# Optimization experiments

Hardware: AMD Instinct MI355X
Metric: run time of the kernel (lower is better)

Reference implementation:

```python
import jax, jax.numpy as jnp
import numpy as np

N_HEAD = 12
MIN_SIZE = 4
MAX_SIZE = 8
TOP_M = 16
ALPHA = 1.0
EPS = 1e-6
NEG_INF = -1e30


def setup_inputs() -> dict:
    key = jax.random.key(0)
    ks = jax.random.split(key, 4)
    B, T, C = 2, 512, 768
    x = jax.random.normal(ks[0], (B, T, C), jnp.float32)
    w_qkv = jax.random.normal(ks[1], (C, 3 * C), jnp.float32) * (1.0 / np.sqrt(C))
    b_qkv = jnp.zeros((3 * C,), jnp.float32)
    w_proj = jax.random.normal(ks[2], (C, C), jnp.float32) * (1.0 / np.sqrt(C))
    b_proj = jnp.zeros((C,), jnp.float32)
    gate_param = jnp.zeros((), jnp.float32)  # dpp_gate_init = 0.0 -> gate = 0.5
    return {"x": x, "w_qkv": w_qkv, "b_qkv": b_qkv, "w_proj": w_proj,
            "b_proj": b_proj, "gate_param": gate_param}


def _dpp_token(i, q_i, k, v):
    """Greedy DPP subset selection + attention for one query token.
    q_i: [hd], k/v: [T, hd]. Faithful to the torch greedy loop, vectorized
    over candidates with incremental Gram construction (scores only gate the
    discrete selection, so they are computed under stop_gradient, matching
    torch where they only feed Python comparisons)."""
    T, hd = k.shape
    kc = jax.lax.stop_gradient(k)
    qc = jax.lax.stop_gradient(q_i)
    # causal similarity, topk candidates
    sim = jnp.where(jnp.arange(T) <= i, kc @ qc, NEG_INF)
    _, topidx = jax.lax.top_k(sim, TOP_M)  # [M]
    # candidates = top-min(TOP_M, i+1) causal neighbors, excluding i itself
    cand_active = (jnp.arange(TOP_M) < jnp.minimum(TOP_M, i + 1)) & (topidx != i)
    cand_keys = kc[topidx]                              # [M, hd]
    cnorm = jnp.sum(cand_keys * cand_keys, axis=-1)     # [M]

    sel_idx = jnp.zeros((MAX_SIZE,), jnp.int32).at[0].set(i)
    sel_count = jnp.int32(1)
    # initial score: log(det([k_i.k_i]) + eps) / 1**alpha
    cur = jnp.log(jnp.dot(kc[i], kc[i]) + EPS)
    stopped = jnp.bool_(False)
    eye = jnp.eye(MAX_SIZE, dtype=jnp.float32)
    slots = jnp.arange(MAX_SIZE)

    for _ in range(MAX_SIZE - 1):
        rowmask = slots < sel_count                       # [S] current subset rows
        pos = (slots == sel_count).astype(jnp.float32)    # slot for new candidate
        Ksel = kc[sel_idx] * rowmask[:, None].astype(jnp.float32)  # [S, hd]
        G0 = Ksel @ Ksel.T                                # [S, S]
        cross = cand_keys @ Ksel.T                        # [M, S]
        # Gc[c,a,b] = G0[a,b] + pos[a]*cross[c,b] + pos[b]*cross[c,a] + pos[a]pos[b]*cnorm[c]
        Gc = (G0[None]
              + pos[None, :, None] * cross[:, None, :]
              + pos[None, None, :] * cross[:, :, None]
              + (pos[:, None] * pos[None, :])[None] * cnorm[:, None, None])
        newmask = rowmask | (slots == sel_count)
        # identity-pad unused rows/cols so det equals det of the active submatrix
        Gc = Gc + (eye * (1.0 - newmask.astype(jnp.float32)))[None]
        dets = jnp.linalg.det(Gc)                         # [M] (float32, as torch)
        size = (sel_count + 1).astype(jnp.float32)
        score = jnp.log(dets + EPS) / size ** ALPHA       # minimize_det=False
        masked = jnp.where(cand_active, score, NEG_INF)
        best = jnp.argmax(masked)
        best_score = masked[best]
        any_cand = jnp.any(cand_active)
        take = any_cand & (~stopped) & ((best_score > cur) | (sel_count < MIN_SIZE))
        sel_idx = jnp.where(take, sel_idx.at[sel_count].set(topidx[best].astype(jnp.int32)), sel_idx)
        cand_active = jnp.where(take, cand_active.at[best].set(False), cand_active)
        cur = jnp.where(take, best_score, cur)
        sel_count = sel_count + take.astype(jnp.int32)
        stopped = stopped | (~take)

    # attention over the selected subset (gradients flow through k, v, q here)
    rowmask = slots < sel_count
    Ks = k[sel_idx]
    Vs = v[sel_idx]
    logits = jnp.where(rowmask, (Ks @ q_i) / np.float32(np.sqrt(hd)), NEG_INF)
    w = jax.nn.softmax(logits)
    return w @ Vs


def _forward(x, w_qkv, b_qkv, w_proj, b_proj, gate_param):
    B, T, C = x.shape
    hd = C // N_HEAD
    qkv = x @ w_qkv + b_qkv
    q, k, v = jnp.split(qkv, 3, axis=-1)

    def heads(t):  # [B,T,C] -> [B*NH, T, hd]
        return t.reshape(B, T, N_HEAD, hd).transpose(0, 2, 1, 3).reshape(B * N_HEAD, T, hd)

    q, k, v = heads(q), heads(k), heads(v)

    # standard causal softmax attention (flash path, dropout=0 at eval)
    scale = np.float32(1.0 / np.sqrt(hd))
    att = jnp.einsum('nqd,nkd->nqk', q, k) * scale
    causal = jnp.tril(jnp.ones((T, T), bool))
    att = jnp.where(causal[None], att, NEG_INF)
    y_std = jnp.einsum('nqk,nkd->nqd', jax.nn.softmax(att, axis=-1), v)

    # DPP greedy-selection attention, vmapped over tokens and (batch*head)
    dpp_head = jax.vmap(_dpp_token, in_axes=(0, 0, None, None))
    y_dpp = jax.vmap(lambda qh, kh, vh: dpp_head(jnp.arange(T), qh, kh, vh))(q, k, v)

    gate = jax.nn.sigmoid(gate_param)
    y = gate * y_dpp + (1.0 - gate) * y_std
    y = y.reshape(B, N_HEAD, T, hd).transpose(0, 2, 1, 3).reshape(B, T, C)
    return y @ w_proj + b_proj


def reference(x, w_qkv, b_qkv, w_proj, b_proj, gate_param):
    return _forward(x, w_qkv, b_qkv, w_proj, b_proj, gate_param)
```

## Files before the change

### kernel.cpp

```cpp
#include <hip/hip_runtime.h>
#include <math.h>

constexpr int SEQ   = 512;
constexpr int HDIM  = 64;
constexpr int NHEAD = 12;
constexpr int NBATCH = 2;
constexpr int CDIM  = 768;
constexpr int TOPM  = 16;
constexpr int SMAX  = 8;
constexpr float NEGINF = -1e30f;

__global__ __launch_bounds__(256) void qkv_gemm_kernel(
    const float* __restrict__ x, const float* __restrict__ w,
    float* __restrict__ partial)
{
    __shared__ float As[128][36];
    __shared__ float Bs[32][68];
    const int bm = blockIdx.y * 128;
    const int bn = blockIdx.x * 64;
    const int kbase = blockIdx.z * 192;
    const int tid = threadIdx.x;
    const int tm = (tid >> 4) << 3;
    const int tn = (tid & 15) << 2;
    const int blk = tid >> 3;
    const int bln = (tid & 7) << 3;
    float acc[8][4] = {};
    for (int t = 0; t < 6; ++t) {
        const int k0 = kbase + t * 32;
        float4 av[4];
        #pragma unroll
        for (int l = 0; l < 4; ++l) {
            int idx = tid + l * 256;
            int row = idx >> 3, kq = (idx & 7) << 2;
            av[l] = *(const float4*)(x + (bm + row) * CDIM + k0 + kq);
        }
        float4 b0 = *(const float4*)(w + (k0 + blk) * (3 * CDIM) + bn + bln);
        float4 b1 = *(const float4*)(w + (k0 + blk) * (3 * CDIM) + bn + bln + 4);
        #pragma unroll
        for (int l = 0; l < 4; ++l) {
            int idx = tid + l * 256;
            int row = idx >> 3, kq = (idx & 7) << 2;
            *(float4*)&As[row][kq] = av[l];
        }
        *(float4*)&Bs[blk][bln] = b0;
        *(float4*)&Bs[blk][bln + 4] = b1;
        __syncthreads();
        #pragma unroll
        for (int k4 = 0; k4 < 8; ++k4) {
            float ar[8][4];
            #pragma unroll
            for (int u = 0; u < 8; ++u) {
                float4 a4 = *(const float4*)&As[tm + u][k4 << 2];
                ar[u][0] = a4.x; ar[u][1] = a4.y;
                ar[u][2] = a4.z; ar[u][3] = a4.w;
            }
            #pragma unroll
            for (int j = 0; j < 4; ++j) {
                float4 b4 = *(const float4*)&Bs[(k4 << 2) + j][tn];
                float bb[4] = {b4.x, b4.y, b4.z, b4.w};
                #pragma unroll
                for (int u = 0; u < 8; ++u)
                    #pragma unroll
                    for (int w2 = 0; w2 < 4; ++w2)
                        acc[u][w2] = fmaf(ar[u][j], bb[w2], acc[u][w2]);
            }
        }
        __syncthreads();
    }
    float* dst = partial + (size_t)blockIdx.z * (1024 * 2304);
    #pragma unroll
    for (int u = 0; u < 8; ++u) {
        float4 o = {acc[u][0], acc[u][1], acc[u][2], acc[u][3]};
        *(float4*)(dst + (size_t)(bm + tm + u) * 2304 + bn + tn) = o;
    }
}

__global__ __launch_bounds__(256) void qkv_reduce_kernel(
    const float* __restrict__ partial, const float* __restrict__ bias,
    float* __restrict__ q, float* __restrict__ k, float* __restrict__ v)
{
    const int idx = blockIdx.x * 256 + threadIdx.x;
    const int m = idx / 576;
    const int cc = (idx - m * 576) << 2;
    const size_t MN = (size_t)1024 * 2304;
    float4 p0 = *(const float4*)(partial + (size_t)m * 2304 + cc);
    float4 p1 = *(const float4*)(partial + MN + (size_t)m * 2304 + cc);
    float4 p2 = *(const float4*)(partial + 2 * MN + (size_t)m * 2304 + cc);
    float4 p3 = *(const float4*)(partial + 3 * MN + (size_t)m * 2304 + cc);
    float4 b4 = *(const float4*)(bias + cc);
    float4 o = {((p0.x + p1.x) + p2.x) + p3.x + b4.x,
                ((p0.y + p1.y) + p2.y) + p3.y + b4.y,
                ((p0.z + p1.z) + p2.z) + p3.z + b4.z,
                ((p0.w + p1.w) + p2.w) + p3.w + b4.w};
    const int part = cc / CDIM;
    const int c2 = cc - part * CDIM;
    const int h = c2 >> 6, d = c2 & 63;
    const int b_ = m >> 9, t = m & 511;
    float* dst = (part == 0) ? q : ((part == 1) ? k : v);
    *(float4*)(dst + ((((size_t)b_ * NHEAD + h) * SEQ) + t) * HDIM + d) = o;
}

__global__ __launch_bounds__(256) void qkkt_kernel(
    const float* __restrict__ q, const float* __restrict__ k,
    float* __restrict__ S, float* __restrict__ KKT)
{
    __shared__ float Qs[64][68];
    __shared__ float Ka[64][68];
    __shared__ float Kb[64][68];
    const int e = blockIdx.x;
    const int n = blockIdx.y;
    int it = 0, start = 0;
    while (start + it + 1 <= e) { start += it + 1; ++it; }
    const int jt = e - start;
    const int tid = threadIdx.x;
    const float* qh = q + (size_t)n * SEQ * HDIM;
    const float* kh = k + (size_t)n * SEQ * HDIM;

    #pragma unroll
    for (int l = 0; l < 4; ++l) {
        int idx = tid + l * 256;
        int tok = idx >> 4, d4 = (idx & 15) << 2;
        *(float4*)&Qs[tok][d4] = *(const float4*)(qh + (it * 64 + tok) * HDIM + d4);
        *(float4*)&Ka[tok][d4] = *(const float4*)(kh + (it * 64 + tok) * HDIM + d4);
        *(float4*)&Kb[tok][d4] = *(const float4*)(kh + (jt * 64 + tok) * HDIM + d4);
    }
    __syncthreads();

    const int tm = (tid >> 4) << 2;
    const int tn = (tid & 15) << 2;
    float sacc[4][4] = {};
    float gacc[4][4] = {};
    #pragma unroll 4
    for (int d4 = 0; d4 < 16; ++d4) {
        float4 qr[4], ar[4], br[4];
        #pragma unroll
        for (int u = 0; u < 4; ++u) {
            qr[u] = *(const float4*)&Qs[tm + u][d4 << 2];
            ar[u] = *(const float4*)&Ka[tm + u][d4 << 2];
        }
        #pragma unroll
        for (int w2 = 0; w2 < 4; ++w2)
            br[w2] = *(const float4*)&Kb[tn + w2][d4 << 2];
        #pragma unroll
        for (int u = 0; u < 4; ++u)
            #pragma unroll
            for (int w2 = 0; w2 < 4; ++w2) {
                float s = sacc[u][w2];
                s = fmaf(qr[u].x, br[w2].x, s);
                s = fmaf(qr[u].y, br[w2].y, s);
                s = fmaf(qr[u].z, br[w2].z, s);
                s = fmaf(qr[u].w, br[w2].w, s);
                sacc[u][w2] = s;
                float g = gacc[u][w2];
                g = fmaf(ar[u].x, br[w2].x, g);
                g = fmaf(ar[u].y, br[w2].y, g);
                g = fmaf(ar[u].z, br[w2].z, g);
                g = fmaf(ar[u].w, br[w2].w, g);
                gacc[u][w2] = g;
            }
    }
    float* gdst = KKT + ((size_t)n * 36 + e) * 4096;
    #pragma unroll
    for (int u = 0; u < 4; ++u) {
        int i = it * 64 + tm + u;
        float4 o = {sacc[u][0], sacc[u][1], sacc[u][2], sacc[u][3]};
        *(float4*)(S + ((size_t)n * SEQ + i) * SEQ + jt * 64 + tn) = o;
        float4 g = {gacc[u][0], gacc[u][1], gacc[u][2], gacc[u][3]};
        *(float4*)(gdst + (tm + u) * 64 + tn) = g;
    }
}

__device__ inline double hybrid_log(double a)
{
    unsigned long long b = __double_as_longlong(a);
    int e2 = (int)((b >> 52) & 0x7FF) - 1022;
    double m = __longlong_as_double((b & 0x000FFFFFFFFFFFFFULL) |
                                    0x3FE0000000000000ULL);
    return ((double)__log2f((float)m) + (double)e2) * 0.6931471805599453;
}

__device__ inline double rsqrt64(double x)
{
    double r = (double)rsqrtf((float)x);
    r = r * (1.5 - 0.5 * x * r * r);
    return r;
}

#define CSW(a, b)                                                        \
    {                                                                    \
        bool sw = (v##a < v##b) || ((v##a == v##b) && (j##a > j##b));    \
        float tf = sw ? v##b : v##a;                                     \
        float uf = sw ? v##a : v##b;                                     \
        int ti = sw ? j##b : j##a;                                       \
        int ui = sw ? j##a : j##b;                                       \
        v##a = tf; v##b = uf; j##a = ti; j##b = ui;                      \
    }

__global__ __launch_bounds__(128) void dpp_kernel(
    const float* __restrict__ v, float* __restrict__ S,
    const float* __restrict__ KKT, const float* __restrict__ gate_p,
    float* __restrict__ y, float* __restrict__ denomArr)
{
    const int tid  = threadIdx.x;
    const int wid  = tid >> 6;
    const int lane = tid & 63;
    const int i = blockIdx.x * 2 + wid;
    const int n = blockIdx.y;
    const float* vh = v + (size_t)n * SEQ * HDIM;
    const float* KKTh = KKT + (size_t)n * 36 * 4096;
    float* Srow = S + ((size_t)n * SEQ + i) * SEQ;

    __shared__ float prow[2][SEQ];
    __shared__ float gramf[2][17][17];
    __shared__ int   eidx[2][17];
    __shared__ int   selS[2][SMAX];

    float sim8[8];
    #pragma unroll
    for (int m = 0; m < 8; ++m) {
        int j = lane + (m << 6);
        sim8[m] = (j <= i) ? Srow[j] : NEGINF;
    }
    if (lane < SMAX) selS[wid][lane] = i;

    {
        float v0 = sim8[0], v1 = sim8[1], v2 = sim8[2], v3 = sim8[3],
              v4 = sim8[4], v5 = sim8[5], v6 = sim8[6], v7 = sim8[7];
        int j0 = lane, j1 = lane + 64, j2 = lane + 128, j3 = lane + 192,
            j4 = lane + 256, j5 = lane + 320, j6 = lane + 384, j7 = lane + 448;
        CSW(0, 1) CSW(2, 3) CSW(4, 5) CSW(6, 7)
        CSW(0, 2) CSW(1, 3) CSW(4, 6) CSW(5, 7)
        CSW(1, 2) CSW(5, 6)
        CSW(0, 4) CSW(1, 5) CSW(2, 6) CSW(3, 7)
        CSW(2, 4) CSW(3, 5)
        CSW(1, 2) CSW(3, 4) CSW(5, 6)

        if (lane == 0) eidx[wid][0] = i;
        #pragma unroll
        for (int s = 0; s < TOPM; ++s) {
            float rv = v0;
            #pragma unroll
            for (int off = 32; off; off >>= 1)
                rv = fmaxf(rv, __shfl_xor(rv, off));
            unsigned long long tied = __ballot(v0 == rv);
            int ri;
            if (__popcll(tied) == 1) {
                ri = __shfl(j0, (int)__builtin_ctzll(tied));
            } else {
                int cnd = (v0 == rv) ? j0 : 0x7FFFFFFF;
                #pragma unroll
                for (int off = 32; off; off >>= 1)
                    cnd = min(cnd, __shfl_xor(cnd, off));
                ri = cnd;
            }
            if (lane == 0) eidx[wid][1 + s] = ri;
            if (v0 == rv && j0 == ri) {
                v0 = v1; j0 = j1; v1 = v2; j1 = j2; v2 = v3; j2 = j3;
                v3 = v4; j3 = j4; v4 = v5; j4 = j5; v5 = v6; j5 = j6;
                v6 = v7; j6 = j7; v7 = -3e38f; j7 = 1023;
            }
        }
    }

    const float scale = 0.125f;
    float lm = -3e38f;
    #pragma unroll
    for (int m = 0; m < 8; ++m) lm = fmaxf(lm, sim8[m]);
    #pragma unroll
    for (int off = 32; off; off >>= 1) lm = fmaxf(lm, __shfl_xor(lm, off));
    const float mx = lm * scale;
    float sum = 0.f;
    #pragma unroll
    for (int m = 0; m < 8; ++m) {
        float p = expf(sim8[m] * scale - mx);
        int j = lane + (m << 6);
        prow[wid][j] = p;
        Srow[j] = p;
        sum += p;
    }
    #pragma unroll
    for (int off = 32; off; off >>= 1) sum += __shfl_xor(sum, off);
    const float denom = sum;
    asm volatile("s_waitcnt lgkmcnt(0)" ::: "memory");

    for (int e = lane; e < 153; e += 64) {
        int a = (int)((sqrtf(8.f * (float)e + 1.f) - 1.f) * 0.5f);
        int st = (a * (a + 1)) >> 1;
        if (st > e) { --a; st = (a * (a + 1)) >> 1; }
        else if (st + a + 1 <= e) { ++a; st = (a * (a + 1)) >> 1; }
        int b = e - st;
        int ra = eidx[wid][a], rb = eidx[wid][b];
        int row = ra > rb ? ra : rb;
        int col = ra > rb ? rb : ra;
        int itt = row >> 6, jtt = col >> 6;
        int p = ((itt * (itt + 1)) >> 1) + jtt;
        float s = KKTh[((size_t)p * 64 + (row & 63)) * 64 + (col & 63)];
        gramf[wid][a][b] = s;
        gramf[wid][b][a] = s;
    }
    asm volatile("s_waitcnt lgkmcnt(0)" ::: "memory");

    int sc = 1;
    {
        const int c = lane;
        const bool isCand = (c < TOPM);
        const int nvalid = (i + 1 < TOPM) ? (i + 1) : TOPM;
        bool active = isCand && (c < nvalid) && (eidx[wid][1 + c] != i);
        double zc[7];
        #pragma unroll
        for (int t = 0; t < 7; ++t) zc[t] = 0.0;
        double det = (double)gramf[wid][0][0];
        double cur = 0.0;
        double invL00 = rsqrt64(det > 0.0 ? det : 1e-30);
        double dcv = 0.0;
        if (isCand) {
            zc[0] = (double)gramf[wid][1 + c][0] * invL00;
            dcv = (double)gramf[wid][1 + c][1 + c] - zc[0] * zc[0];
        }

        for (int it2 = 0; it2 < SMAX - 1; ++it2) {
            double argc = det * dcv + 1e-6;
            double key = active ? (argc > 0.0 ? argc : 1e300) : -1.0;
            int rc = c;
            #pragma unroll
            for (int off = 1; off <= 8; off <<= 1) {
                double ov = __shfl_xor(key, off);
                int    oc = __shfl_xor(rc, off);
                if (ov > key || (ov == key && oc < rc)) { key = ov; rc = oc; }
            }
            rc = __shfl(rc, 0);
            bool any = (__any(active ? 1 : 0) != 0);
            double dbest = __shfl(dcv, rc);
            bool take;
            if (it2 < 2) {
                take = any;
            } else {
                double argb = det * dbest + 1e-6;
                bool pos = argb > 0.0;
                double score = hybrid_log(pos ? argb : 1.0) / (double)(sc + 1);
                take = any && (it2 < 3 || (pos && score > cur));
                if (take) cur = pos ? score : __builtin_nan("");
            }
            if (!take) break;

            double invLss = rsqrt64(dbest > 1e-30 ? dbest : 1e-30);
            double zb[7];
            #pragma unroll
            for (int t = 0; t < 7; ++t) zb[t] = __shfl(zc[t], rc);
            if (isCand) {
                double crossn = (double)gramf[wid][1 + c][1 + rc];
                double s2 = 0.0;
                #pragma unroll
                for (int t = 0; t < 7; ++t) s2 += zc[t] * zb[t];
                double znew = (crossn - s2) * invLss;
                #pragma unroll
                for (int t = 0; t < 7; ++t) if (t == sc) zc[t] = znew;
                dcv -= znew * znew;
            }
            det = det * dbest;
            if (c == rc) active = false;
            if (lane == 0) selS[wid][sc] = eidx[wid][1 + rc];
            ++sc;
        }
    }

    int selI[SMAX];
    #pragma unroll
    for (int s = 0; s < SMAX; ++s) selI[s] = selS[wid][s];
    float wsum = 0.f;
    #pragma unroll
    for (int s = 0; s < SMAX; ++s) if (s < sc) wsum += prow[wid][selI[s]];
    float yd = 0.f;
    #pragma unroll
    for (int s = 0; s < SMAX; ++s)
        if (s < sc) yd = fmaf(prow[wid][selI[s]], vh[selI[s] * HDIM + lane], yd);
    const float gp = gate_p[0];
    const float gate = 1.f / (1.f + expf(-gp));
    y[((size_t)n * SEQ + i) * HDIM + lane] = gate * yd / wsum;
    if (lane == 0) denomArr[n * SEQ + i] = denom;
}

__global__ __launch_bounds__(256) void pv_gemm_kernel(
    const float* __restrict__ P, const float* __restrict__ v,
    const float* __restrict__ denomArr, const float* __restrict__ gate_p,
    float* __restrict__ y)
{
    __shared__ float Ps[32][36];
    __shared__ float Vs[32][68];
    const int tt = blockIdx.x;
    const int n  = blockIdx.y;
    const int t0 = tt * 32;
    const int tid = threadIdx.x;
    const float* Ph = P + (size_t)n * SEQ * SEQ;
    const float* vh = v + (size_t)n * SEQ * HDIM;
    const int tm = (tid >> 4) << 1;
    const int tn = (tid & 15) << 2;
    float acc[2][4] = {};
    const int jmax = t0 + 32;
    for (int j0 = 0; j0 < jmax; j0 += 32) {
        {
            int tok = tid >> 3, j4 = (tid & 7) << 2;
            *(float4*)&Ps[tok][j4] =
                *(const float4*)(Ph + (t0 + tok) * SEQ + j0 + j4);
        }
        #pragma unroll
        for (int l = 0; l < 2; ++l) {
            int idx = tid + l * 256;
            int j = idx >> 4, d4 = (idx & 15) << 2;
            *(float4*)&Vs[j][d4] = *(const float4*)(vh + (j0 + j) * HDIM + d4);
        }
        __syncthreads();
        #pragma unroll
        for (int j4 = 0; j4 < 8; ++j4) {
            float4 p0r = *(const float4*)&Ps[tm + 0][j4 << 2];
            float4 p1r = *(const float4*)&Ps[tm + 1][j4 << 2];
            float pr[2][4] = {{p0r.x, p0r.y, p0r.z, p0r.w},
                              {p1r.x, p1r.y, p1r.z, p1r.w}};
            #pragma unroll
            for (int l = 0; l < 4; ++l) {
                float4 v4 = *(const float4*)&Vs[(j4 << 2) + l][tn];
                float vv[4] = {v4.x, v4.y, v4.z, v4.w};
                #pragma unroll
                for (int u = 0; u < 2; ++u)
                    #pragma unroll
                    for (int w2 = 0; w2 < 4; ++w2)
                        acc[u][w2] = fmaf(pr[u][l], vv[w2], acc[u][w2]);
            }
        }
        __syncthreads();
    }
    const float gp = gate_p[0];
    const float gate = 1.f / (1.f + expf(-gp));
    #pragma unroll
    for (int u = 0; u < 2; ++u) {
        int i = t0 + tm + u;
        float den = denomArr[n * SEQ + i];
        #pragma unroll
        for (int w2 = 0; w2 < 4; ++w2) {
            int d = tn + w2;
            size_t off = ((size_t)n * SEQ + i) * HDIM + d;
            y[off] += (1.f - gate) * acc[u][w2] / den;
        }
    }
}

__global__ __launch_bounds__(256) void proj_gemm_kernel(
    const float* __restrict__ y, const float* __restrict__ w,
    float* __restrict__ partial)
{
    __shared__ float As[128][36];
    __shared__ float Bs[32][68];
    const int bm = blockIdx.y * 128;
    const int bn = blockIdx.x * 64;
    const int kbase = blockIdx.z * 96;
    const int tid = threadIdx.x;
    const int tm = (tid >> 4) << 3;
    const int tn = (tid & 15) << 2;
    const int blk = tid >> 3;
    const int bln = (tid & 7) << 3;

    float acc[8][4] = {};
    for (int t = 0; t < 3; ++t) {
        const int k0 = kbase + t * 32;
        float4 av[4];
        #pragma unroll
        for (int l = 0; l < 4; ++l) {
            int idx = tid + l * 256;
            int row = bm + (idx >> 3);
            int col = k0 + ((idx & 7) << 2);
            int b_ = row >> 9, tk = row & 511;
            int h = col >> 6, d = col & 63;
            av[l] = *(const float4*)(y + ((((size_t)b_ * NHEAD + h) * SEQ) + tk) * HDIM + d);
        }
        float4 b0 = *(const float4*)(w + (k0 + blk) * CDIM + bn + bln);
        float4 b1 = *(const float4*)(w + (k0 + blk) * CDIM + bn + bln + 4);
        #pragma unroll
        for (int l = 0; l < 4; ++l) {
            int idx = tid + l * 256;
            int row = idx >> 3, kq = (idx & 7) << 2;
            *(float4*)&As[row][kq] = av[l];
        }
        *(float4*)&Bs[blk][bln] = b0;
        *(float4*)&Bs[blk][bln + 4] = b1;
        __syncthreads();
        #pragma unroll
        for (int k4 = 0; k4 < 8; ++k4) {
            float ar[8][4];
            #pragma unroll
            for (int u = 0; u < 8; ++u) {
                float4 a4 = *(const float4*)&As[tm + u][k4 << 2];
                ar[u][0] = a4.x; ar[u][1] = a4.y;
                ar[u][2] = a4.z; ar[u][3] = a4.w;
            }
            #pragma unroll
            for (int j = 0; j < 4; ++j) {
                float4 b4 = *(const float4*)&Bs[(k4 << 2) + j][tn];
                float bb[4] = {b4.x, b4.y, b4.z, b4.w};
                #pragma unroll
                for (int u = 0; u < 8; ++u)
                    #pragma unroll
                    for (int w2 = 0; w2 < 4; ++w2)
                        acc[u][w2] = fmaf(ar[u][j], bb[w2], acc[u][w2]);
            }
        }
        __syncthreads();
    }
    float* dst = partial + (size_t)blockIdx.z * (1024 * 768);
    #pragma unroll
    for (int u = 0; u < 8; ++u) {
        float4 o = {acc[u][0], acc[u][1], acc[u][2], acc[u][3]};
        *(float4*)(dst + (size_t)(bm + tm + u) * 768 + bn + tn) = o;
    }
}

__global__ __launch_bounds__(256) void proj_reduce_kernel(
    const float* __restrict__ partial, const float* __restrict__ bias,
    float* __restrict__ out)
{
    const int idx = blockIdx.x * 256 + threadIdx.x;
    const int m = idx / 192;
    const int cc = (idx - m * 192) << 2;
    const size_t MN = (size_t)1024 * 768;
    float4 s = *(const float4*)(partial + (size_t)m * 768 + cc);
    #pragma unroll
    for (int z = 1; z < 8; ++z) {
        float4 p = *(const float4*)(partial + (size_t)z * MN + (size_t)m * 768 + cc);
        s.x += p.x; s.y += p.y; s.z += p.z; s.w += p.w;
    }
    float4 b4 = *(const float4*)(bias + cc);
    float4 o = {s.x + b4.x, s.y + b4.y, s.z + b4.z, s.w + b4.w};
    *(float4*)(out + (size_t)m * 768 + cc) = o;
}

extern "C" void kernel_launch(void* const* d_in, const int* in_sizes, int n_in,
                              void* d_out, int out_size, void* d_ws, size_t ws_size,
                              hipStream_t stream)
{
    const float* x      = (const float*)d_in[0];
    const float* w_qkv  = (const float*)d_in[1];
    const float* b_qkv  = (const float*)d_in[2];
    const float* w_proj = (const float*)d_in[3];
    const float* b_proj = (const float*)d_in[4];
    const float* gate_p = (const float*)d_in[5];
    float* out = (float*)d_out;

    float* ws = (float*)d_ws;
    const size_t HS = (size_t)NBATCH * NHEAD * SEQ * HDIM;
    const size_t SS = (size_t)NBATCH * NHEAD * SEQ * SEQ;
    float* q   = ws;
    float* k   = q + HS;
    float* v   = k + HS;
    float* y   = v + HS;
    float* S   = y + HS;
    float* den = S + SS;
    float* KKT = den + 16384;

    qkv_gemm_kernel<<<dim3((3 * CDIM) / 64, (NBATCH * SEQ) / 128, 4), 256, 0, stream>>>(
        x, w_qkv, S);
    qkv_reduce_kernel<<<2304, 256, 0, stream>>>(S, b_qkv, q, k, v);
    qkkt_kernel<<<dim3(36, NBATCH * NHEAD), 256, 0, stream>>>(q, k, S, KKT);
    dpp_kernel<<<dim3(SEQ / 2, NBATCH * NHEAD), 128, 0, stream>>>(
        v, S, KKT, gate_p, y, den);
    pv_gemm_kernel<<<dim3(SEQ / 32, NBATCH * NHEAD), 256, 0, stream>>>(
        S, v, den, gate_p, y);
    proj_gemm_kernel<<<dim3(CDIM / 64, (NBATCH * SEQ) / 128, 8), 256, 0, stream>>>(
        y, w_proj, S);
    proj_reduce_kernel<<<768, 256, 0, stream>>>(S, b_proj, out);
}
```

Baseline: 183.1 us.

## Load QKV GEMM tiles directly into LDS with XOR swizzle and smaller blocks

The QKV GEMM now uses global_load_lds to copy 16-byte chunks from global memory straight into shared memory, skipping the trip through registers. The A tile uses an XOR swizzle in place of padding to avoid bank conflicts. The block tile shrinks from 128x64 to 64x64 with 128 threads, which doubles the grid and should improve occupancy and overlap. The risk is that the direct-to-LDS layout must match the swizzled reads exactly, and smaller tiles reuse each loaded operand less.

```diff
diff --git a/kernel.cpp b/kernel.cpp
--- a/kernel.cpp
+++ b/kernel.cpp
@@ -10,53 +10,60 @@
 constexpr int SMAX  = 8;
 constexpr float NEGINF = -1e30f;
 
-__global__ __launch_bounds__(256) void qkv_gemm_kernel(
+__device__ inline void gload_lds16(const float* src, float* lds_base)
+{
+    __builtin_amdgcn_global_load_lds(
+        (const __attribute__((address_space(1))) void*)src,
+        (__attribute__((address_space(3))) void*)lds_base, 16, 0, 0);
+}
+
+__global__ __launch_bounds__(128) void qkv_gemm_kernel(
     const float* __restrict__ x, const float* __restrict__ w,
     float* __restrict__ partial)
 {
-    __shared__ float As[128][36];
-    __shared__ float Bs[32][68];
-    const int bm = blockIdx.y * 128;
+    __shared__ float As[64 * 32];
+    __shared__ float Bs[32 * 64];
+    const int bm = blockIdx.y * 64;
     const int bn = blockIdx.x * 64;
     const int kbase = blockIdx.z * 192;
     const int tid = threadIdx.x;
+    const int wid = tid >> 6;
     const int tm = (tid >> 4) << 3;
     const int tn = (tid & 15) << 2;
-    const int blk = tid >> 3;
-    const int bln = (tid & 7) << 3;
+    const int swzA = ((tid >> 4) & 3) << 2;
     float acc[8][4] = {};
     for (int t = 0; t < 6; ++t) {
         const int k0 = kbase + t * 32;
-        float4 av[4];
         #pragma unroll
         for (int l = 0; l < 4; ++l) {
-            int idx = tid + l * 256;
-            int row = idx >> 3, kq = (idx & 7) << 2;
-            av[l] = *(const float4*)(x + (bm + row) * CDIM + k0 + kq);
-        }
-        float4 b0 = *(const float4*)(w + (k0 + blk) * (3 * CDIM) + bn + bln);
-        float4 b1 = *(const float4*)(w + (k0 + blk) * (3 * CDIM) + bn + bln + 4);
+            int slot = l * 128 + tid;
+            int row = slot >> 3;
+            int kq = (slot & 7) << 2;
+            int kqs = kq ^ (((row >> 3) & 3) << 2);
+            gload_lds16(x + (bm + row) * CDIM + k0 + kqs,
+                        As + (l * 128 + wid * 64) * 4);
+        }
         #pragma unroll
         for (int l = 0; l < 4; ++l) {
-            int idx = tid + l * 256;
-            int row = idx >> 3, kq = (idx & 7) << 2;
-            *(float4*)&As[row][kq] = av[l];
-        }
-        *(float4*)&Bs[blk][bln] = b0;
-        *(float4*)&Bs[blk][bln + 4] = b1;
+            int slot = l * 128 + tid;
+            int kk = slot >> 4;
+            int col = (slot & 15) << 2;
+            gload_lds16(w + (k0 + kk) * (3 * CDIM) + bn + col,
+                        Bs + (l * 128 + wid * 64) * 4);
+        }
         __syncthreads();
         #pragma unroll
         for (int k4 = 0; k4 < 8; ++k4) {
             float ar[8][4];
             #pragma unroll
             for (int u = 0; u < 8; ++u) {
-                float4 a4 = *(const float4*)&As[tm + u][k4 << 2];
+                float4 a4 = *(const float4*)(As + (tm + u) * 32 + ((k4 << 2) ^ swzA));
                 ar[u][0] = a4.x; ar[u][1] = a4.y;
                 ar[u][2] = a4.z; ar[u][3] = a4.w;
             }
             #pragma unroll
             for (int j = 0; j < 4; ++j) {
-                float4 b4 = *(const float4*)&Bs[(k4 << 2) + j][tn];
+                float4 b4 = *(const float4*)(Bs + ((k4 << 2) + j) * 64 + tn);
                 float bb[4] = {b4.x, b4.y, b4.z, b4.w};
                 #pragma unroll
                 for (int u = 0; u < 8; ++u)
@@ -555,7 +562,7 @@
     float* den = S + SS;
     float* KKT = den + 16384;
 
-    qkv_gemm_kernel<<<dim3((3 * CDIM) / 64, (NBATCH * SEQ) / 128, 4), 256, 0, stream>>>(
+    qkv_gemm_kernel<<<dim3((3 * CDIM) / 64, (NBATCH * SEQ) / 64, 4), 128, 0, stream>>>(
         x, w_qkv, S);
     qkv_reduce_kernel<<<2304, 256, 0, stream>>>(S, b_qkv, q, k, v);
     qkkt_kernel<<<dim3(36, NBATCH * NHEAD), 256, 0, stream>>>(q, k, S, KKT);
```

New measurement: 182.9 us. About the same (-0.1%).
